# Kernel tuning notes

Hardware: AMD Instinct MI355X
Metric: run time of the kernel (lower is better)

The kernel has to match this reference:

```python
import jax, jax.numpy as jnp
import numpy as np


def setup_inputs() -> dict:
    key = jax.random.key(0)
    k1, k2, k3 = jax.random.split(key, 3)
    B, C, H, W, F, K = 8, 32, 64, 64, 64, 3
    x = jax.random.normal(k1, (B, C, H, W), dtype=jnp.float32)
    # per-weight rational (safe Pade [5/4]) coefficients: one activation per (f, a, b, c)
    num_coef = jax.random.normal(k2, (F, K, K, C, 6), dtype=jnp.float32) * 0.1
    den_coef = jax.random.normal(k3, (F, K, K, C, 4), dtype=jnp.float32) * 0.1
    return {"x": x, "num_coef": num_coef, "den_coef": den_coef}


def _rational(x, an, bd):
    """Safe Pade rational: P(x)/(1+|x*(b1+x*(b2+x*(b3+x*b4)))|).
    x: [B,H,W,K,K,C]; an: [K,K,C,6]; bd: [K,K,C,4] (broadcast over B,H,W)."""
    num = an[..., 5]
    for i in (4, 3, 2, 1, 0):  # Horner, ascending coeff order a0..a5
        num = num * x + an[..., i]
    q = bd[..., 3]
    for i in (2, 1, 0):
        q = q * x + bd[..., i]
    den = 1.0 + jnp.abs(q * x)
    return num / den


def reference(x, num_coef, den_coef):
    B, C, H, W = x.shape
    F, K = num_coef.shape[0], num_coef.shape[1]
    p = (K - 1) // 2
    xp = jnp.pad(x, ((0, 0), (0, 0), (p, p), (p, p)))  # zero pad H,W
    xp = jnp.transpose(xp, (0, 2, 3, 1))  # [B, H+2p, W+2p, C]
    # im2col patches: [B, H, W, K, K, C]
    patches = jnp.stack(
        [jnp.stack([xp[:, a:a + H, b:b + W, :] for b in range(K)], axis=3)
         for a in range(K)], axis=3)

    def per_filter(coefs):
        an, bd = coefs  # [K,K,C,6], [K,K,C,4]
        y = _rational(patches, an, bd)  # [B,H,W,K,K,C]
        return jnp.sum(y, axis=(3, 4, 5))  # [B,H,W]

    out = jax.lax.map(per_filter, (num_coef, den_coef))  # [F,B,H,W]
    return jnp.transpose(out, (1, 0, 2, 3))  # [B,F,H,W]
```

## Files before the change

kernel.cpp:

```cpp
#include <hip/hip_runtime.h>


typedef int   iv4  __attribute__((ext_vector_type(4)));
typedef short s8v  __attribute__((ext_vector_type(8)));
typedef float f16v __attribute__((ext_vector_type(16)));

#define Bb 8
#define Cc 32
#define Hh 64
#define Ww 64
#define Ff 64
#define PW 66
#define PPLANE (PW * PW)
#define NELEM  (Bb * Cc * PPLANE)
#define NTAP   288
#define ABLK   (NTAP * 4 * 64 / 256)
#define PW2BLK (NELEM / 512)

static __device__ __forceinline__ unsigned short f2h(float f) {
    return __builtin_bit_cast(unsigned short, (_Float16)f);
}
static __device__ __forceinline__ int pack2(unsigned short a, unsigned short b) {
    return (int)((unsigned)a | ((unsigned)b << 16));
}
static __device__ __forceinline__ iv4 ld16(const char* p) {
    return *(const iv4* __restrict__)p;
}

__global__ __launch_bounds__(256) void prep_kernel(
    const float* __restrict__ x,
    const float* __restrict__ ncf, const float* __restrict__ dcf,
    iv4* __restrict__ pw, iv4* __restrict__ ac)
{
    if ((int)blockIdx.x < ABLK) {
        int tidx = (int)blockIdx.x * 256 + (int)threadIdx.x;
        if (tidx == 0) { iv4 z = {0, 0, 0, 0}; pw[NELEM] = z; }
        int l    = tidx / 1152;
        int rem  = tidx - l * 1152;
        int tile = rem / 288;
        int t    = rem - tile * 288;
        int m = l & 31;
        float cv[6];
        if (tile < 2) {
            int f = tile * 32 + m;
            const float2* s2 = (const float2*)(ncf + ((size_t)f * NTAP + t) * 6);
            float2 a01 = s2[0], a23 = s2[1], a45 = s2[2];
            cv[0] = a01.x; cv[1] = a01.y; cv[2] = a23.x;
            cv[3] = a23.y; cv[4] = a45.x; cv[5] = a45.y;
        } else {
            int f = (tile - 2) * 32 + m;
            const float4* s4 = (const float4*)(dcf + ((size_t)f * NTAP + t) * 4);
            float4 b03 = s4[0];
            cv[0] = 0.0f; cv[1] = b03.x; cv[2] = b03.y;
            cv[3] = b03.z; cv[4] = b03.w; cv[5] = 0.0f;
        }
        iv4 o;
        o.x = pack2(f2h(cv[0]), f2h(cv[1]));
        o.y = pack2(f2h(cv[2]), f2h(cv[3]));
        o.z = pack2(f2h(cv[4]), f2h(cv[5]));
        o.w = 0;
        ac[((size_t)t * 4 + tile) * 64 + l] = o;
    } else {
        int base = ((int)blockIdx.x - ABLK) * 512 + (int)threadIdx.x;
#pragma unroll
        for (int half = 0; half < 2; ++half) {
            int idx = base + half * 256;
            int wp = idx % PW;
            int r1 = idx / PW;
            int hp = r1 % PW;
            int pl = r1 / PW;
            float v = 0.0f;
            if (hp >= 1 && hp <= Hh && wp >= 1 && wp <= Ww)
                v = x[((size_t)pl * Hh + (hp - 1)) * Ww + (wp - 1)];
            float p2 = v * v, p3 = p2 * v, p4 = p2 * p2, p5 = p4 * v;
            iv4 r0;
            r0.x = pack2((unsigned short)0x3C00, f2h(v));
            r0.y = pack2(f2h(p2), f2h(p3));
            r0.z = pack2(f2h(p4), f2h(p5));
            r0.w = 0;
            pw[idx] = r0;
        }
    }
}

__global__ __launch_bounds__(256, 4) void kan_mfma_kernel(
    const iv4* __restrict__ pw, const iv4* __restrict__ ac,
    float* __restrict__ out)
{
    const int tid = threadIdx.x;
    const int l = tid & 63, v = tid >> 6, ln = l & 31, g = l >> 5;
    const int gb = (int)blockIdx.x;
    const int wh = gb & 1, h = (gb >> 1) & 63, bb = gb >> 7;
    const int w0 = wh << 5;

    __shared__ float red[4][64][33];

    f16v acc0, acc1, zf;
#pragma unroll
    for (int r = 0; r < 16; ++r) { acc0[r] = 0.0f; acc1[r] = 0.0f; zf[r] = 0.0f; }

    const char* __restrict__ pwc = (const char*)pw;
    const unsigned baseB = (g == 0) ? 0u : (unsigned)NELEM * 16u;
    const unsigned mE    = (g == 0) ? 0xFFFFFFFFu : 0u;

    const int tEnd = v * 72 + 72;
#pragma unroll 1
    for (int t = v * 72; t < tEnd; ++t) {
        const int c = t & 31, k2 = t >> 5;
        const int dy = k2 / 3, dx = k2 - dy * 3;
        const int elem = ((bb * Cc + c) * PW + (h + dy)) * PW + (w0 + ln + dx);
        iv4 bl = ld16(pwc + (baseB + (((unsigned)(elem * 16)) & mE)));
        const iv4* ap = ac + (size_t)t * 256;
        iv4 A0 = ap[l], A1 = ap[64 + l], A2 = ap[128 + l], A3 = ap[192 + l];
        s8v bF = __builtin_bit_cast(s8v, bl);

        f16v D0 = __builtin_amdgcn_mfma_f32_32x32x16_f16(
            __builtin_bit_cast(s8v, A0), bF, zf, 0, 0, 0);
        f16v D2 = __builtin_amdgcn_mfma_f32_32x32x16_f16(
            __builtin_bit_cast(s8v, A2), bF, zf, 0, 0, 0);
#pragma unroll
        for (int r = 0; r < 16; ++r) {
            float dd = 1.0f + __builtin_fabsf(D2[r]);
            float rc = __builtin_amdgcn_rcpf(dd);
            acc0[r] = __builtin_fmaf(D0[r], rc, acc0[r]);
        }
        f16v D1 = __builtin_amdgcn_mfma_f32_32x32x16_f16(
            __builtin_bit_cast(s8v, A1), bF, zf, 0, 0, 0);
        f16v D3 = __builtin_amdgcn_mfma_f32_32x32x16_f16(
            __builtin_bit_cast(s8v, A3), bF, zf, 0, 0, 0);
#pragma unroll
        for (int r = 0; r < 16; ++r) {
            float dd = 1.0f + __builtin_fabsf(D3[r]);
            float rc = __builtin_amdgcn_rcpf(dd);
            acc1[r] = __builtin_fmaf(D1[r], rc, acc1[r]);
        }
    }

#pragma unroll
    for (int r = 0; r < 16; ++r) {
        red[v][l][r]      = acc0[r];
        red[v][l][16 + r] = acc1[r];
    }
    __syncthreads();

#pragma unroll
    for (int jj = 0; jj < 8; ++jj) {
        int j = v * 8 + jj;
        float s = red[0][l][j] + red[1][l][j] + red[2][l][j] + red[3][l][j];
        int tt = j >> 4, r = j & 15;
        int f = tt * 32 + (r & 3) + ((r >> 2) << 3) + ((l >> 5) << 2);
        out[(((size_t)bb * Ff + f) * Hh + h) * Ww + w0 + ln] = s;
    }
}

extern "C" void kernel_launch(void* const* d_in, const int* in_sizes, int n_in,
                              void* d_out, int out_size, void* d_ws, size_t ws_size,
                              hipStream_t stream) {
    const float* x   = (const float*)d_in[0];
    const float* ncf = (const float*)d_in[1];
    const float* dcf = (const float*)d_in[2];
    float* out = (float*)d_out;

    iv4* pw = (iv4*)d_ws;
    iv4* ac = pw + NELEM + 1;

    prep_kernel<<<ABLK + PW2BLK, 256, 0, stream>>>(x, ncf, dcf, pw, ac);
    kan_mfma_kernel<<<1024, 256, 0, stream>>>(pw, ac, out);
}
```

Measured before the change: 151.0 us.

## Compute x power vectors in-register from padded fp32 instead of precomputed fp16 table

The prep kernel now writes only a zero-padded fp32 copy of x instead of a 16-byte-per-element table of fp16 powers. The main kernel loads one float per tap and builds the MFMA B operand in registers, computing powers up to x^5 and packing them with cvt_pkrtz. The upper lane half is zeroed by multiplying by a mask rather than by redirecting its load to a zero sentinel. The block index mapping is also reordered so batch varies fastest, which changes L2 locality. Together these cut prep writes and main-loop load bytes by about 4x, at the cost of extra ALU work per tap and round-toward-zero fp16 conversion instead of round-to-nearest.

After: 147.7 us. -2.2%, faster.

```diff
diff --git a/kernel.cpp b/kernel.cpp
--- a/kernel.cpp
+++ b/kernel.cpp
@@ -1,9 +1,10 @@
 #include <hip/hip_runtime.h>
 
 
-typedef int   iv4  __attribute__((ext_vector_type(4)));
-typedef short s8v  __attribute__((ext_vector_type(8)));
-typedef float f16v __attribute__((ext_vector_type(16)));
+typedef int    iv4 __attribute__((ext_vector_type(4)));
+typedef short  s8v __attribute__((ext_vector_type(8)));
+typedef float  f16v __attribute__((ext_vector_type(16)));
+typedef __fp16 h2v __attribute__((ext_vector_type(2)));
 
 #define Bb 8
 #define Cc 32
@@ -15,7 +16,7 @@
 #define NELEM  (Bb * Cc * PPLANE)
 #define NTAP   288
 #define ABLK   (NTAP * 4 * 64 / 256)
-#define PW2BLK (NELEM / 512)
+#define PADBLK (NELEM / 512)
 
 static __device__ __forceinline__ unsigned short f2h(float f) {
     return __builtin_bit_cast(unsigned short, (_Float16)f);
@@ -23,18 +24,14 @@
 static __device__ __forceinline__ int pack2(unsigned short a, unsigned short b) {
     return (int)((unsigned)a | ((unsigned)b << 16));
 }
-static __device__ __forceinline__ iv4 ld16(const char* p) {
-    return *(const iv4* __restrict__)p;
-}
 
 __global__ __launch_bounds__(256) void prep_kernel(
     const float* __restrict__ x,
     const float* __restrict__ ncf, const float* __restrict__ dcf,
-    iv4* __restrict__ pw, iv4* __restrict__ ac)
+    float* __restrict__ xpad, iv4* __restrict__ ac)
 {
     if ((int)blockIdx.x < ABLK) {
         int tidx = (int)blockIdx.x * 256 + (int)threadIdx.x;
-        if (tidx == 0) { iv4 z = {0, 0, 0, 0}; pw[NELEM] = z; }
         int l    = tidx / 1152;
         int rem  = tidx - l * 1152;
         int tile = rem / 288;
@@ -72,25 +69,19 @@
             float v = 0.0f;
             if (hp >= 1 && hp <= Hh && wp >= 1 && wp <= Ww)
                 v = x[((size_t)pl * Hh + (hp - 1)) * Ww + (wp - 1)];
-            float p2 = v * v, p3 = p2 * v, p4 = p2 * p2, p5 = p4 * v;
-            iv4 r0;
-            r0.x = pack2((unsigned short)0x3C00, f2h(v));
-            r0.y = pack2(f2h(p2), f2h(p3));
-            r0.z = pack2(f2h(p4), f2h(p5));
-            r0.w = 0;
-            pw[idx] = r0;
+            xpad[idx] = v;
         }
     }
 }
 
 __global__ __launch_bounds__(256, 4) void kan_mfma_kernel(
-    const iv4* __restrict__ pw, const iv4* __restrict__ ac,
+    const float* __restrict__ xpad, const iv4* __restrict__ ac,
     float* __restrict__ out)
 {
     const int tid = threadIdx.x;
     const int l = tid & 63, v = tid >> 6, ln = l & 31, g = l >> 5;
     const int gb = (int)blockIdx.x;
-    const int wh = gb & 1, h = (gb >> 1) & 63, bb = gb >> 7;
+    const int bb = gb & 7, h = (gb >> 3) & 63, wh = (gb >> 9) & 1;
     const int w0 = wh << 5;
 
     __shared__ float red[4][64][33];
@@ -99,9 +90,7 @@
 #pragma unroll
     for (int r = 0; r < 16; ++r) { acc0[r] = 0.0f; acc1[r] = 0.0f; zf[r] = 0.0f; }
 
-    const char* __restrict__ pwc = (const char*)pw;
-    const unsigned baseB = (g == 0) ? 0u : (unsigned)NELEM * 16u;
-    const unsigned mE    = (g == 0) ? 0xFFFFFFFFu : 0u;
+    const float mk = (g == 0) ? 1.0f : 0.0f;
 
     const int tEnd = v * 72 + 72;
 #pragma unroll 1
@@ -109,7 +98,18 @@
         const int c = t & 31, k2 = t >> 5;
         const int dy = k2 / 3, dx = k2 - dy * 3;
         const int elem = ((bb * Cc + c) * PW + (h + dy)) * PW + (w0 + ln + dx);
-        iv4 bl = ld16(pwc + (baseB + (((unsigned)(elem * 16)) & mE)));
+
+        float xv = xpad[elem] * mk;
+        float p2 = xv * xv, p3 = p2 * xv, p4 = p2 * p2, p5 = p4 * xv;
+        h2v pk0 = __builtin_amdgcn_cvt_pkrtz(mk, xv);
+        h2v pk1 = __builtin_amdgcn_cvt_pkrtz(p2, p3);
+        h2v pk2 = __builtin_amdgcn_cvt_pkrtz(p4, p5);
+        iv4 bl;
+        bl.x = (int)__builtin_bit_cast(unsigned, pk0);
+        bl.y = (int)__builtin_bit_cast(unsigned, pk1);
+        bl.z = (int)__builtin_bit_cast(unsigned, pk2);
+        bl.w = 0;
+
         const iv4* ap = ac + (size_t)t * 256;
         iv4 A0 = ap[l], A1 = ap[64 + l], A2 = ap[128 + l], A3 = ap[192 + l];
         s8v bF = __builtin_bit_cast(s8v, bl);
@@ -161,9 +161,9 @@
     const float* dcf = (const float*)d_in[2];
     float* out = (float*)d_out;
 
-    iv4* pw = (iv4*)d_ws;
-    iv4* ac = pw + NELEM + 1;
+    float* xpad = (float*)d_ws;
+    iv4*   ac   = (iv4*)(xpad + NELEM);
 
-    prep_kernel<<<ABLK + PW2BLK, 256, 0, stream>>>(x, ncf, dcf, pw, ac);
-    kan_mfma_kernel<<<1024, 256, 0, stream>>>(pw, ac, out);
+    prep_kernel<<<ABLK + PADBLK, 256, 0, stream>>>(x, ncf, dcf, xpad, ac);
+    kan_mfma_kernel<<<1024, 256, 0, stream>>>(xpad, ac, out);
 }
```
